# Kernel optimization log

Measured on AMD Instinct MI355X. Metric: run time of the kernel, lower is better.

## Reference

```python
import jax, jax.numpy as jnp
import numpy as np

N_TREES, DEPTH, INPUT_DIM, N_CLASSES = 15, 3, 128, 10
N_LEAVES = 2 ** DEPTH
N_INTERNAL = N_LEAVES - 1


def _path_masks(depth):
    """Right/left ancestor indicator matrices [n_leaves, n_internal]."""
    n_leaves = 2 ** depth
    n_int = n_leaves - 1
    R = np.zeros((n_leaves, n_int), np.float32)
    L = np.zeros((n_leaves, n_int), np.float32)
    for leaf in range(n_leaves):
        node = leaf + n_int
        for _ in range(depth):
            parent = (node - 1) // 2
            if node % 2 == 0:
                R[leaf, parent] = 1.0
            else:
                L[leaf, parent] = 1.0
            node = parent
    return R, L

_R, _L = _path_masks(DEPTH)


def setup_inputs() -> dict:
    key = jax.random.key(0)
    k1, k2 = jax.random.split(key)
    batch = 262144
    per_tree = N_INTERNAL * INPUT_DIM + N_INTERNAL + N_LEAVES * N_CLASSES
    total = N_TREES * per_tree + N_TREES
    x = jax.random.normal(k1, (batch, INPUT_DIM), dtype=jnp.float32)
    params = jax.random.normal(k2, (total,), dtype=jnp.float32)
    return {"x": x, "params": params}


def reference(x, params):
    per_tree = N_INTERNAL * INPUT_DIM + N_INTERNAL + N_LEAVES * N_CLASSES
    blocks = params[: N_TREES * per_tree].reshape(N_TREES, per_tree)
    w_end = N_INTERNAL * INPUT_DIM
    split_w = blocks[:, :w_end].reshape(N_TREES, N_INTERNAL, INPUT_DIM)
    split_b = blocks[:, w_end : w_end + N_INTERNAL]  # [T, n_internal]
    leaf_logits = blocks[:, w_end + N_INTERNAL :].reshape(N_TREES, N_LEAVES, N_CLASSES)
    tree_w_logits = params[N_TREES * per_tree :]  # [T]

    # split logits z: [B, T, n_internal]
    z = jnp.einsum("bd,tnd->btn", x, split_w) + split_b[None, :, :]
    log_p = jax.nn.log_sigmoid(z)        # log sigma(z)
    log_1mp = jax.nn.log_sigmoid(-z)     # log (1 - sigma(z))

    R = jnp.asarray(_R)
    L = jnp.asarray(_L)
    # path product in log domain: [B, T, n_leaves]
    leaf_probs = jnp.exp(
        jnp.einsum("btn,ln->btl", log_p, R) + jnp.einsum("btn,ln->btl", log_1mp, L)
    )

    leaf_class_probs = jax.nn.softmax(leaf_logits, axis=-1)  # [T, n_leaves, C]
    tree_pred = jnp.einsum("btl,tlc->btc", leaf_probs, leaf_class_probs)
    tree_weights = jax.nn.softmax(tree_w_logits, axis=0)     # [T]
    final_pred = jnp.einsum("btc,t->bc", tree_pred, tree_weights)
    return final_pred
```

## Files before the change

kernel.cpp:

```cpp
#include <hip/hip_runtime.h>
#include <hip/hip_fp16.h>


typedef float  f32x4 __attribute__((ext_vector_type(4)));
typedef _Float16 half8 __attribute__((ext_vector_type(8)));

#define TREES      15
#define IDIM       128
#define NCLS       10
#define NINT       7
#define NLVS       8
#define PER_TREE   (NINT*IDIM + NINT + NLVS*NCLS)
#define NODES      (TREES*NINT)
#define NPAD       112
#define STR        113
#define MROWS      128
#define WLC_N      (TREES*NLVS*NCLS)

__global__ __launch_bounds__(256) void prep_kernel(const float* __restrict__ p,
                                                   __half* __restrict__ wq,
                                                   float* __restrict__ bq,
                                                   float* __restrict__ wlc) {
    int tid = threadIdx.x;
    for (int i = tid; i < NPAD * IDIM; i += 256) {
        int g = i >> 7, k = i & 127;
        float v = 0.f;
        if (g < NODES) {
            int t = g / NINT, n = g % NINT;
            v = p[t * PER_TREE + n * IDIM + k];
        }
        wq[i] = __float2half(v);
    }
    for (int i = tid; i < NPAD; i += 256) {
        float v = 0.f;
        if (i < NODES) {
            int t = i / NINT, n = i % NINT;
            v = p[t * PER_TREE + NINT * IDIM + n];
        }
        bq[i] = v;
    }
    const float* tl = p + TREES * PER_TREE;
    for (int i = tid; i < WLC_N; i += 256) {
        int t = i / (NLVS * NCLS);
        int l = (i / NCLS) % NLVS;
        int c = i % NCLS;
        const float* ll = p + t * PER_TREE + NINT * IDIM + NINT + l * NCLS;
        float mx = ll[0];
        #pragma unroll
        for (int j = 1; j < NCLS; ++j) mx = fmaxf(mx, ll[j]);
        float se = 0.f;
        #pragma unroll
        for (int j = 0; j < NCLS; ++j) se += __expf(ll[j] - mx);
        float lsm = __expf(ll[c] - mx) / se;

        float m2 = tl[0];
        #pragma unroll
        for (int j = 1; j < TREES; ++j) m2 = fmaxf(m2, tl[j]);
        float s2 = 0.f;
        #pragma unroll
        for (int j = 0; j < TREES; ++j) s2 += __expf(tl[j] - m2);
        float tw = __expf(tl[t] - m2) / s2;

        wlc[i] = lsm * tw;
    }
}

__global__ __launch_bounds__(256, 4) void tree_main(const float* __restrict__ x,
                                                    const __half* __restrict__ wq,
                                                    const float* __restrict__ bq,
                                                    const float* __restrict__ wlc,
                                                    float* __restrict__ out) {
    __shared__ __half s_sh[MROWS * STR];
    __shared__ float  wlc_sh[WLC_N];
    __shared__ float  out_sh[MROWS * NCLS];

    const int tid  = threadIdx.x;
    const int lane = tid & 63;
    const int wave = tid >> 6;
    const int lm   = lane & 15;
    const int lq   = lane >> 4;

    for (int i = tid; i < WLC_N; i += 256) wlc_sh[i] = wlc[i];

    const int T0 = wave;
    const int T1 = wave + 4;
    const bool two = (T1 < 7);
    half8 bf0[4], bf1[4];
    float bb0, bb1 = 0.f;
    bb0 = bq[16 * T0 + lm];
    #pragma unroll
    for (int s = 0; s < 4; ++s)
        bf0[s] = *reinterpret_cast<const half8*>(wq + (16 * T0 + lm) * IDIM + 32 * s + 8 * lq);
    if (two) {
        bb1 = bq[16 * T1 + lm];
        #pragma unroll
        for (int s = 0; s < 4; ++s)
            bf1[s] = *reinterpret_cast<const half8*>(wq + (16 * T1 + lm) * IDIM + 32 * s + 8 * lq);
    }

    const long base_row = (long)blockIdx.x * MROWS;

    for (int mt = 0; mt < 8; ++mt) {
        const float* xr = x + (base_row + mt * 16 + lm) * IDIM + 8 * lq;
        half8 af[4];
        #pragma unroll
        for (int s = 0; s < 4; ++s) {
            f32x4 f0 = *reinterpret_cast<const f32x4*>(xr + 32 * s);
            f32x4 f1 = *reinterpret_cast<const f32x4*>(xr + 32 * s + 4);
            half8 a;
            #pragma unroll
            for (int j = 0; j < 4; ++j) {
                a[j]     = (_Float16)f0[j];
                a[j + 4] = (_Float16)f1[j];
            }
            af[s] = a;
        }

        f32x4 acc0 = {0.f, 0.f, 0.f, 0.f};
        #pragma unroll
        for (int s = 0; s < 4; ++s)
            acc0 = __builtin_amdgcn_mfma_f32_16x16x32_f16(af[s], bf0[s], acc0, 0, 0, 0);
        {
            const int colbase = 16 * T0 + lm;
            #pragma unroll
            for (int r = 0; r < 4; ++r) {
                float z = acc0[r] + bb0;
                float sg = 1.0f / (1.0f + __expf(-z));
                s_sh[(mt * 16 + lq * 4 + r) * STR + colbase] = __float2half(sg);
            }
        }
        if (two) {
            f32x4 acc1 = {0.f, 0.f, 0.f, 0.f};
            #pragma unroll
            for (int s = 0; s < 4; ++s)
                acc1 = __builtin_amdgcn_mfma_f32_16x16x32_f16(af[s], bf1[s], acc1, 0, 0, 0);
            const int colbase = 16 * T1 + lm;
            #pragma unroll
            for (int r = 0; r < 4; ++r) {
                float z = acc1[r] + bb1;
                float sg = 1.0f / (1.0f + __expf(-z));
                s_sh[(mt * 16 + lq * 4 + r) * STR + colbase] = __float2half(sg);
            }
        }
    }
    __syncthreads();

    const int row = tid >> 1;
    const int h   = tid & 1;
    const __half* sr = s_sh + row * STR;
    float acc[NCLS];
    #pragma unroll
    for (int c = 0; c < NCLS; ++c) acc[c] = 0.f;

    const int t_beg = h ? 8 : 0;
    const int t_end = h ? 15 : 8;
    for (int t = t_beg; t < t_end; ++t) {
        const __half* sn = sr + t * NINT;
        float s0 = __half2float(sn[0]);
        float s1 = __half2float(sn[1]);
        float s2 = __half2float(sn[2]);
        float s3 = __half2float(sn[3]);
        float s4 = __half2float(sn[4]);
        float s5 = __half2float(sn[5]);
        float s6 = __half2float(sn[6]);
        float u1 = 1.f - s0, u2 = s0;
        float q1 = u1 * s1, q0 = u1 - q1;
        float q3 = u2 * s2, q2 = u2 - q3;
        float L1 = q0 * s3, L0 = q0 - L1;
        float L3 = q1 * s4, L2 = q1 - L3;
        float L5 = q2 * s5, L4 = q2 - L5;
        float L7 = q3 * s6, L6 = q3 - L7;
        const float* wl = wlc_sh + t * (NLVS * NCLS);
        #pragma unroll
        for (int c = 0; c < NCLS; ++c) {
            float a = L0 * wl[c]       + L1 * wl[NCLS + c]
                    + L2 * wl[2*NCLS+c] + L3 * wl[3*NCLS+c]
                    + L4 * wl[4*NCLS+c] + L5 * wl[5*NCLS+c]
                    + L6 * wl[6*NCLS+c] + L7 * wl[7*NCLS+c];
            acc[c] += a;
        }
    }
    #pragma unroll
    for (int c = 0; c < NCLS; ++c) acc[c] += __shfl_xor(acc[c], 1, 64);
    if (!h) {
        #pragma unroll
        for (int c = 0; c < NCLS; ++c) out_sh[row * NCLS + c] = acc[c];
    }
    __syncthreads();

    const long ob = (long)blockIdx.x * (MROWS * NCLS);
    for (int i = tid; i < MROWS * NCLS; i += 256) out[ob + i] = out_sh[i];
}

extern "C" void kernel_launch(void* const* d_in, const int* in_sizes, int n_in,
                              void* d_out, int out_size, void* d_ws, size_t ws_size,
                              hipStream_t stream) {
    const float* x      = (const float*)d_in[0];
    const float* params = (const float*)d_in[1];
    float* out = (float*)d_out;

    __half* wq  = (__half*)d_ws;
    float*  bq  = (float*)((char*)d_ws + NPAD * IDIM * 2);
    float*  wlc = bq + NPAD;

    const int batch  = in_sizes[0] / IDIM;
    const int blocks = batch / MROWS;

    prep_kernel<<<1, 256, 0, stream>>>(params, wq, bq, wlc);
    tree_main<<<blocks, 256, 0, stream>>>(x, wq, bq, wlc, out);
}
```

Before: 251.3 us.

## Compute leaf-to-class mixing with MFMA instead of scalar FMA loops

The final stage, which mixes leaf probabilities with the weighted leaf-class table, now runs as a 128x128 by 128x16 fp16 MFMA GEMM. Before, each thread did scalar FMAs per tree with float weights held in shared memory. Leaf probabilities are computed per row from vectorized shared reads, written back as fp16 into the same shared buffer, and consumed as MFMA A-fragments. The prep kernel now builds a transposed, padded fp16 class-weight matrix and runs on 8 blocks, and the sigmoid uses a hardware reciprocal. This cuts ALU work and shared-memory traffic and drops the output staging buffer, at the cost of fp16 precision for the leaf probabilities and weights and an extra barrier.

```diff
diff --git a/kernel.cpp b/kernel.cpp
--- a/kernel.cpp
+++ b/kernel.cpp
@@ -2,7 +2,7 @@
 #include <hip/hip_fp16.h>
 
 
-typedef float  f32x4 __attribute__((ext_vector_type(4)));
+typedef float    f32x4 __attribute__((ext_vector_type(4)));
 typedef _Float16 half8 __attribute__((ext_vector_type(8)));
 
 #define TREES      15
@@ -13,25 +13,27 @@
 #define PER_TREE   (NINT*IDIM + NINT + NLVS*NCLS)
 #define NODES      (TREES*NINT)
 #define NPAD       112
-#define STR        113
 #define MROWS      128
-#define WLC_N      (TREES*NLVS*NCLS)
+#define LSTR       136
+#define KPAD       128
 
 __global__ __launch_bounds__(256) void prep_kernel(const float* __restrict__ p,
-                                                   __half* __restrict__ wq,
+                                                   _Float16* __restrict__ wq,
                                                    float* __restrict__ bq,
-                                                   float* __restrict__ wlc) {
-    int tid = threadIdx.x;
-    for (int i = tid; i < NPAD * IDIM; i += 256) {
+                                                   _Float16* __restrict__ wbT) {
+    const int gid = blockIdx.x * 256 + threadIdx.x;
+    const int nthr = gridDim.x * 256;
+
+    for (int i = gid; i < NPAD * IDIM; i += nthr) {
         int g = i >> 7, k = i & 127;
         float v = 0.f;
         if (g < NODES) {
             int t = g / NINT, n = g % NINT;
             v = p[t * PER_TREE + n * IDIM + k];
         }
-        wq[i] = __float2half(v);
-    }
-    for (int i = tid; i < NPAD; i += 256) {
+        wq[i] = (_Float16)v;
+    }
+    for (int i = gid; i < NPAD; i += nthr) {
         float v = 0.f;
         if (i < NODES) {
             int t = i / NINT, n = i % NINT;
@@ -40,39 +42,39 @@
         bq[i] = v;
     }
     const float* tl = p + TREES * PER_TREE;
-    for (int i = tid; i < WLC_N; i += 256) {
-        int t = i / (NLVS * NCLS);
-        int l = (i / NCLS) % NLVS;
-        int c = i % NCLS;
-        const float* ll = p + t * PER_TREE + NINT * IDIM + NINT + l * NCLS;
-        float mx = ll[0];
-        #pragma unroll
-        for (int j = 1; j < NCLS; ++j) mx = fmaxf(mx, ll[j]);
-        float se = 0.f;
-        #pragma unroll
-        for (int j = 0; j < NCLS; ++j) se += __expf(ll[j] - mx);
-        float lsm = __expf(ll[c] - mx) / se;
-
-        float m2 = tl[0];
-        #pragma unroll
-        for (int j = 1; j < TREES; ++j) m2 = fmaxf(m2, tl[j]);
-        float s2 = 0.f;
-        #pragma unroll
-        for (int j = 0; j < TREES; ++j) s2 += __expf(tl[j] - m2);
-        float tw = __expf(tl[t] - m2) / s2;
-
-        wlc[i] = lsm * tw;
+    for (int i = gid; i < 16 * KPAD; i += nthr) {
+        int c = i >> 7, k = i & 127;
+        float v = 0.f;
+        if (c < NCLS && k < TREES * NLVS) {
+            int t = k >> 3, l = k & 7;
+            const float* ll = p + t * PER_TREE + NINT * IDIM + NINT + l * NCLS;
+            float mx = ll[0];
+            #pragma unroll
+            for (int j = 1; j < NCLS; ++j) mx = fmaxf(mx, ll[j]);
+            float se = 0.f;
+            #pragma unroll
+            for (int j = 0; j < NCLS; ++j) se += __expf(ll[j] - mx);
+            float lsm = __expf(ll[c] - mx) / se;
+
+            float m2 = tl[0];
+            #pragma unroll
+            for (int j = 1; j < TREES; ++j) m2 = fmaxf(m2, tl[j]);
+            float s2 = 0.f;
+            #pragma unroll
+            for (int j = 0; j < TREES; ++j) s2 += __expf(tl[j] - m2);
+            float tw = __expf(tl[t] - m2) / s2;
+            v = lsm * tw;
+        }
+        wbT[i] = (_Float16)v;
     }
 }
 
 __global__ __launch_bounds__(256, 4) void tree_main(const float* __restrict__ x,
-                                                    const __half* __restrict__ wq,
+                                                    const _Float16* __restrict__ wq,
                                                     const float* __restrict__ bq,
-                                                    const float* __restrict__ wlc,
+                                                    const _Float16* __restrict__ wbT,
                                                     float* __restrict__ out) {
-    __shared__ __half s_sh[MROWS * STR];
-    __shared__ float  wlc_sh[WLC_N];
-    __shared__ float  out_sh[MROWS * NCLS];
+    __shared__ _Float16 s_sh[MROWS * LSTR];
 
     const int tid  = threadIdx.x;
     const int lane = tid & 63;
@@ -80,19 +82,16 @@
     const int lm   = lane & 15;
     const int lq   = lane >> 4;
 
-    for (int i = tid; i < WLC_N; i += 256) wlc_sh[i] = wlc[i];
-
     const int T0 = wave;
     const int T1 = wave + 4;
     const bool two = (T1 < 7);
     half8 bf0[4], bf1[4];
-    float bb0, bb1 = 0.f;
-    bb0 = bq[16 * T0 + lm];
+    float bb0 = bq[16 * T0 + lm];
+    float bb1 = two ? bq[16 * T1 + lm] : 0.f;
     #pragma unroll
     for (int s = 0; s < 4; ++s)
         bf0[s] = *reinterpret_cast<const half8*>(wq + (16 * T0 + lm) * IDIM + 32 * s + 8 * lq);
     if (two) {
-        bb1 = bq[16 * T1 + lm];
         #pragma unroll
         for (int s = 0; s < 4; ++s)
             bf1[s] = *reinterpret_cast<const half8*>(wq + (16 * T1 + lm) * IDIM + 32 * s + 8 * lq);
@@ -124,9 +123,9 @@
             const int colbase = 16 * T0 + lm;
             #pragma unroll
             for (int r = 0; r < 4; ++r) {
-                float z = acc0[r] + bb0;
-                float sg = 1.0f / (1.0f + __expf(-z));
-                s_sh[(mt * 16 + lq * 4 + r) * STR + colbase] = __float2half(sg);
+                float z  = acc0[r] + bb0;
+                float sg = __builtin_amdgcn_rcpf(1.0f + __expf(-z));
+                s_sh[(mt * 16 + lq * 4 + r) * LSTR + colbase] = (_Float16)sg;
             }
         }
         if (two) {
@@ -137,59 +136,85 @@
             const int colbase = 16 * T1 + lm;
             #pragma unroll
             for (int r = 0; r < 4; ++r) {
-                float z = acc1[r] + bb1;
-                float sg = 1.0f / (1.0f + __expf(-z));
-                s_sh[(mt * 16 + lq * 4 + r) * STR + colbase] = __float2half(sg);
+                float z  = acc1[r] + bb1;
+                float sg = __builtin_amdgcn_rcpf(1.0f + __expf(-z));
+                s_sh[(mt * 16 + lq * 4 + r) * LSTR + colbase] = (_Float16)sg;
             }
         }
     }
     __syncthreads();
 
-    const int row = tid >> 1;
-    const int h   = tid & 1;
-    const __half* sr = s_sh + row * STR;
-    float acc[NCLS];
-    #pragma unroll
-    for (int c = 0; c < NCLS; ++c) acc[c] = 0.f;
-
-    const int t_beg = h ? 8 : 0;
-    const int t_end = h ? 15 : 8;
-    for (int t = t_beg; t < t_end; ++t) {
-        const __half* sn = sr + t * NINT;
-        float s0 = __half2float(sn[0]);
-        float s1 = __half2float(sn[1]);
-        float s2 = __half2float(sn[2]);
-        float s3 = __half2float(sn[3]);
-        float s4 = __half2float(sn[4]);
-        float s5 = __half2float(sn[5]);
-        float s6 = __half2float(sn[6]);
-        float u1 = 1.f - s0, u2 = s0;
-        float q1 = u1 * s1, q0 = u1 - q1;
-        float q3 = u2 * s2, q2 = u2 - q3;
-        float L1 = q0 * s3, L0 = q0 - L1;
-        float L3 = q1 * s4, L2 = q1 - L3;
-        float L5 = q2 * s5, L4 = q2 - L5;
-        float L7 = q3 * s6, L6 = q3 - L7;
-        const float* wl = wlc_sh + t * (NLVS * NCLS);
-        #pragma unroll
-        for (int c = 0; c < NCLS; ++c) {
-            float a = L0 * wl[c]       + L1 * wl[NCLS + c]
-                    + L2 * wl[2*NCLS+c] + L3 * wl[3*NCLS+c]
-                    + L4 * wl[4*NCLS+c] + L5 * wl[5*NCLS+c]
-                    + L6 * wl[6*NCLS+c] + L7 * wl[7*NCLS+c];
-            acc[c] += a;
-        }
-    }
-    #pragma unroll
-    for (int c = 0; c < NCLS; ++c) acc[c] += __shfl_xor(acc[c], 1, 64);
-    if (!h) {
-        #pragma unroll
-        for (int c = 0; c < NCLS; ++c) out_sh[row * NCLS + c] = acc[c];
+    {
+        const int row = tid & 127;
+        const int h   = tid >> 7;
+        const _Float16* sr = s_sh + row * LSTR + 56 * h;
+        half8 sv[8];
+        #pragma unroll
+        for (int j = 0; j < 8; ++j)
+            sv[j] = *reinterpret_cast<const half8*>(sr + 8 * j);
+
+        half8 leafv[8];
+        #pragma unroll
+        for (int tt = 0; tt < 8; ++tt) {
+            if (h == 1 && tt == 7) {
+                half8 zz = {(_Float16)0.f, (_Float16)0.f, (_Float16)0.f, (_Float16)0.f,
+                            (_Float16)0.f, (_Float16)0.f, (_Float16)0.f, (_Float16)0.f};
+                leafv[7] = zz;
+            } else {
+                float s0 = (float)sv[(7*tt+0) >> 3][(7*tt+0) & 7];
+                float s1 = (float)sv[(7*tt+1) >> 3][(7*tt+1) & 7];
+                float s2 = (float)sv[(7*tt+2) >> 3][(7*tt+2) & 7];
+                float s3 = (float)sv[(7*tt+3) >> 3][(7*tt+3) & 7];
+                float s4 = (float)sv[(7*tt+4) >> 3][(7*tt+4) & 7];
+                float s5 = (float)sv[(7*tt+5) >> 3][(7*tt+5) & 7];
+                float s6 = (float)sv[(7*tt+6) >> 3][(7*tt+6) & 7];
+                float u1 = 1.f - s0, u2 = s0;
+                float q1 = u1 * s1, q0 = u1 - q1;
+                float q3 = u2 * s2, q2 = u2 - q3;
+                float L1 = q0 * s3, L0 = q0 - L1;
+                float L3 = q1 * s4, L2 = q1 - L3;
+                float L5 = q2 * s5, L4 = q2 - L5;
+                float L7 = q3 * s6, L6 = q3 - L7;
+                half8 lv;
+                lv[0] = (_Float16)L0; lv[1] = (_Float16)L1;
+                lv[2] = (_Float16)L2; lv[3] = (_Float16)L3;
+                lv[4] = (_Float16)L4; lv[5] = (_Float16)L5;
+                lv[6] = (_Float16)L6; lv[7] = (_Float16)L7;
+                leafv[tt] = lv;
+            }
+        }
+        __syncthreads();
+        _Float16* lw = s_sh + row * LSTR + 64 * h;
+        #pragma unroll
+        for (int j = 0; j < 8; ++j)
+            *reinterpret_cast<half8*>(lw + 8 * j) = leafv[j];
     }
     __syncthreads();
 
-    const long ob = (long)blockIdx.x * (MROWS * NCLS);
-    for (int i = tid; i < MROWS * NCLS; i += 256) out[ob + i] = out_sh[i];
+    {
+        half8 wbf[4];
+        #pragma unroll
+        for (int s = 0; s < 4; ++s)
+            wbf[s] = *reinterpret_cast<const half8*>(wbT + lm * KPAD + 32 * s + 8 * lq);
+
+        #pragma unroll
+        for (int u = 0; u < 2; ++u) {
+            const int mt = wave + 4 * u;
+            half8 af[4];
+            #pragma unroll
+            for (int s = 0; s < 4; ++s)
+                af[s] = *reinterpret_cast<const half8*>(s_sh + (16 * mt + lm) * LSTR + 32 * s + 8 * lq);
+            f32x4 acc = {0.f, 0.f, 0.f, 0.f};
+            #pragma unroll
+            for (int s = 0; s < 4; ++s)
+                acc = __builtin_amdgcn_mfma_f32_16x16x32_f16(af[s], wbf[s], acc, 0, 0, 0);
+            if (lm < NCLS) {
+                #pragma unroll
+                for (int r = 0; r < 4; ++r)
+                    out[(base_row + 16 * mt + 4 * lq + r) * NCLS + lm] = acc[r];
+            }
+        }
+    }
 }
 
 extern "C" void kernel_launch(void* const* d_in, const int* in_sizes, int n_in,
@@ -199,13 +224,13 @@
     const float* params = (const float*)d_in[1];
     float* out = (float*)d_out;
 
-    __half* wq  = (__half*)d_ws;
-    float*  bq  = (float*)((char*)d_ws + NPAD * IDIM * 2);
-    float*  wlc = bq + NPAD;
+    _Float16* wq  = (_Float16*)d_ws;
+    float*    bq  = (float*)((char*)d_ws + NPAD * IDIM * 2);
+    _Float16* wbT = (_Float16*)((char*)bq + NPAD * 4);
 
     const int batch  = in_sizes[0] / IDIM;
     const int blocks = batch / MROWS;
 
-    prep_kernel<<<1, 256, 0, stream>>>(params, wq, bq, wlc);
-    tree_main<<<blocks, 256, 0, stream>>>(x, wq, bq, wlc, out);
+    prep_kernel<<<8, 256, 0, stream>>>(params, wq, bq, wbT);
+    tree_main<<<blocks, 256, 0, stream>>>(x, wq, bq, wbT, out);
 }
```

New measurement: 221.6 us. 1.13x faster.
